# Performance work log

Hardware: AMD Instinct MI355X
Metric: run time of the kernel (lower is better)

## Reference

```python
import jax, jax.numpy as jnp
import numpy as np

WIN = 11
K1 = 0.01
K2 = 0.03


def setup_inputs() -> dict:
    key = jax.random.key(0)
    k1, k2 = jax.random.split(key)
    B, C, H, W = 64, 1, 512, 512
    img = jax.random.uniform(k1, (B, C, H, W), dtype=jnp.float32)
    ref = jax.random.uniform(k2, (B, C, H, W), dtype=jnp.float32)
    data_range = jnp.ones((B,), dtype=jnp.float32)
    return {"img": img, "ref": ref, "data_range": data_range}


def _box_filter(x, win):
    w = jnp.ones((1, 1, win, win), dtype=x.dtype) / (win * win)
    pad = win // 2
    return jax.lax.conv_general_dilated(
        x, w, window_strides=(1, 1),
        padding=[(pad, pad), (pad, pad)],
        dimension_numbers=("NCHW", "OIHW", "NCHW"))


def reference(img, ref, data_range):
    dr = data_range[:, None, None, None]
    C1 = (K1 * dr) ** 2
    C2 = (K2 * dr) ** 2
    n_pix = WIN * WIN
    cov_norm = n_pix / (n_pix - 1)

    ux = _box_filter(img, WIN)
    uy = _box_filter(ref, WIN)
    uxx = _box_filter(img * img, WIN)
    uyy = _box_filter(ref * ref, WIN)
    uxy = _box_filter(img * ref, WIN)

    vx = cov_norm * (uxx - ux * ux)
    vy = cov_norm * (uyy - uy * uy)
    vxy = cov_norm * (uxy - ux * uy)

    A1 = 2 * ux * uy + C1
    A2 = 2 * vxy + C2
    B1 = ux ** 2 + uy ** 2 + C1
    B2 = vx + vy + C2
    S = A1 * A2 / (B1 * B2)
    return S
```

## Files before the change

kernel.cpp:

```cpp
#include <hip/hip_runtime.h>


static constexpr int HI = 512, WI = 512;
static constexpr int RS = 8;
static constexpr int STEPS = RS + 10;
static constexpr int SPB = HI / RS;

struct R8 { float4 a, b; };

__device__ __forceinline__ R8 ld8(const float* p) {
  R8 r; r.a = ((const float4*)p)[0]; r.b = ((const float4*)p)[1]; return r;
}

__device__ __forceinline__ void horiz11(const float v[8], float H[8], int lane) {
  float L[5], R[5];
#pragma unroll
  for (int k = 0; k < 5; ++k) {
    float lt = __shfl(v[3 + k], (lane + 63) & 63);
    L[k] = (lane == 0) ? 0.f : lt;
    float rt = __shfl(v[k], (lane + 1) & 63);
    R[k] = (lane == 63) ? 0.f : rt;
  }
  float h = (((L[0] + L[1]) + (L[2] + L[3])) + ((L[4] + v[0]) + (v[1] + v[2])))
            + ((v[3] + v[4]) + v[5]);
  H[0] = h;
  h = h - L[0] + v[6]; H[1] = h;
  h = h - L[1] + v[7]; H[2] = h;
  h = h - L[2] + R[0]; H[3] = h;
  h = h - L[3] + R[1]; H[4] = h;
  h = h - L[4] + R[2]; H[5] = h;
  h = h - v[0] + R[3]; H[6] = h;
  h = h - v[1] + R[4]; H[7] = h;
}

__global__ __launch_bounds__(256, 2)
void ssim_wave(const float* __restrict__ img, const float* __restrict__ ref,
               const float* __restrict__ drng, const float* __restrict__ zrow,
               float* __restrict__ out)
{
  int bid = (int)blockIdx.x;
  const int nb = (int)gridDim.x;
  if ((nb & 7) == 0) {
    const int cpx = nb >> 3;
    bid = (bid & 7) * cpx + (bid >> 3);
  }

  const int lane = threadIdx.x & 63;
  const int wv   = bid * 4 + (threadIdx.x >> 6);
  const int b    = wv / SPB;
  const int r0   = (wv % SPB) * RS;
  const int c0   = lane * 8;

  const float dr  = drng[b];
  const float C1  = (0.01f * dr) * (0.01f * dr);
  const float C2  = (0.03f * dr) * (0.03f * dr);
  const float inv_n    = 1.0f / 121.0f;
  const float cov_norm = 121.0f / 120.0f;

  const size_t base = (size_t)b * ((size_t)HI * WI);
  const float* xb = img + base;
  const float* yb = ref + base;
  float*       ob = out + base;

  auto nptr = [&](const float* tb, int i) -> const float* {
    const int ri = r0 - 5 + i;
    return (((unsigned)ri < (unsigned)HI) ? tb + (size_t)ri * WI : zrow) + c0;
  };
  auto optr = [&](const float* tb, int i) -> const float* {
    const int ro = r0 - 16 + i;
    return ((i >= 11 && ro >= 0) ? tb + (size_t)ro * WI : zrow) + c0;
  };

  float Sx[8], Sy[8], Sxx[8], Syy[8], Sxy[8];
#pragma unroll
  for (int c = 0; c < 8; ++c) { Sx[c]=0.f; Sy[c]=0.f; Sxx[c]=0.f; Syy[c]=0.f; Sxy[c]=0.f; }

  R8 nx[2], ny[2], ox[2], oy[2];
  nx[0]=ld8(nptr(xb,0)); ny[0]=ld8(nptr(yb,0)); ox[0]=ld8(optr(xb,0)); oy[0]=ld8(optr(yb,0));
  nx[1]=ld8(nptr(xb,1)); ny[1]=ld8(nptr(yb,1)); ox[1]=ld8(optr(xb,1)); oy[1]=ld8(optr(yb,1));

#pragma unroll 2
  for (int i = 0; i < STEPS; ++i) {
    const int s = i & 1;
    float xn[8] = { nx[s].a.x, nx[s].a.y, nx[s].a.z, nx[s].a.w,
                    nx[s].b.x, nx[s].b.y, nx[s].b.z, nx[s].b.w };
    float yn[8] = { ny[s].a.x, ny[s].a.y, ny[s].a.z, ny[s].a.w,
                    ny[s].b.x, ny[s].b.y, ny[s].b.z, ny[s].b.w };
    float xo[8] = { ox[s].a.x, ox[s].a.y, ox[s].a.z, ox[s].a.w,
                    ox[s].b.x, ox[s].b.y, ox[s].b.z, ox[s].b.w };
    float yo[8] = { oy[s].a.x, oy[s].a.y, oy[s].a.z, oy[s].a.w,
                    oy[s].b.x, oy[s].b.y, oy[s].b.z, oy[s].b.w };

    if (i + 2 < STEPS) {
      nx[s]=ld8(nptr(xb,i+2)); ny[s]=ld8(nptr(yb,i+2));
      ox[s]=ld8(optr(xb,i+2)); oy[s]=ld8(optr(yb,i+2));
    }

#pragma unroll
    for (int c = 0; c < 8; ++c) {
      Sx[c]  += xn[c] - xo[c];
      Sy[c]  += yn[c] - yo[c];
      Sxx[c] = fmaf(xn[c], xn[c], fmaf(-xo[c], xo[c], Sxx[c]));
      Syy[c] = fmaf(yn[c], yn[c], fmaf(-yo[c], yo[c], Syy[c]));
      Sxy[c] = fmaf(xn[c], yn[c], fmaf(-xo[c], yo[c], Sxy[c]));
    }

    if (i >= 10) {
      float H0[8], H1[8], H2[8], H3[8], H4[8];
      horiz11(Sx,  H0, lane);
      horiz11(Sy,  H1, lane);
      horiz11(Sxx, H2, lane);
      horiz11(Syy, H3, lane);
      horiz11(Sxy, H4, lane);

      float res[8];
#pragma unroll
      for (int c = 0; c < 8; ++c) {
        const float ux  = H0[c] * inv_n, uy  = H1[c] * inv_n;
        const float uxx = H2[c] * inv_n, uyy = H3[c] * inv_n, uxy = H4[c] * inv_n;
        const float vx  = cov_norm * (uxx - ux * ux);
        const float vy  = cov_norm * (uyy - uy * uy);
        const float vxy = cov_norm * (uxy - ux * uy);
        const float A1 = 2.f * ux * uy + C1;
        const float A2 = 2.f * vxy + C2;
        const float B1 = ux * ux + uy * uy + C1;
        const float B2 = vx + vy + C2;
        res[c] = (A1 * A2) * __builtin_amdgcn_rcpf(B1 * B2);
      }
      const int ro = r0 + i - 10;
      float4* po = (float4*)(ob + (size_t)ro * WI + c0);
      po[0] = make_float4(res[0], res[1], res[2], res[3]);
      po[1] = make_float4(res[4], res[5], res[6], res[7]);
    }
  }
}

extern "C" void kernel_launch(void* const* d_in, const int* in_sizes, int n_in,
                              void* d_out, int out_size, void* d_ws, size_t ws_size,
                              hipStream_t stream)
{
  const float* img = (const float*)d_in[0];
  const float* ref = (const float*)d_in[1];
  const float* drg = (const float*)d_in[2];
  float* out = (float*)d_out;

  hipMemsetAsync(d_ws, 0, (size_t)WI * sizeof(float) + 64, stream);

  const int B = in_sizes[0] / (HI * WI);
  const int waves = B * SPB;
  dim3 grid(waves / 4);
  dim3 block(256);
  hipLaunchKernelGGL(ssim_wave, grid, block, 0, stream,
                     img, ref, drg, (const float*)d_ws, out);
}
```

Baseline: 222.6 us.

## Double rows per wave and peel warm-up loop to skip dummy old-row loads

Each wave now produces 16 output rows instead of 8, so the 10-row vertical halo is amortised over more outputs and less input is re-read per output row. The sliding loop is split into a warm-up phase that only accumulates new rows and a steady phase that adds new rows and subtracts old ones. The warm-up phase no longer loads or subtracts zero rows. The grid is halved, which lowers the number of resident waves for hiding latency, and the peeled loop makes the code larger.

```diff
diff --git a/kernel.cpp b/kernel.cpp
--- a/kernel.cpp
+++ b/kernel.cpp
@@ -2,14 +2,18 @@
 
 
 static constexpr int HI = 512, WI = 512;
-static constexpr int RS = 8;
-static constexpr int STEPS = RS + 10;
+static constexpr int RS = 16;
 static constexpr int SPB = HI / RS;
 
 struct R8 { float4 a, b; };
 
 __device__ __forceinline__ R8 ld8(const float* p) {
   R8 r; r.a = ((const float4*)p)[0]; r.b = ((const float4*)p)[1]; return r;
+}
+
+__device__ __forceinline__ void unp(const R8& v, float o[8]) {
+  o[0]=v.a.x; o[1]=v.a.y; o[2]=v.a.z; o[3]=v.a.w;
+  o[4]=v.b.x; o[5]=v.b.y; o[6]=v.b.z; o[7]=v.b.w;
 }
 
 __device__ __forceinline__ void horiz11(const float v[8], float H[8], int lane) {
@@ -62,77 +66,114 @@
   const float* yb = ref + base;
   float*       ob = out + base;
 
-  auto nptr = [&](const float* tb, int i) -> const float* {
-    const int ri = r0 - 5 + i;
-    return (((unsigned)ri < (unsigned)HI) ? tb + (size_t)ri * WI : zrow) + c0;
+  auto nrow = [&](const float* tb, int t) -> const float* {
+    const int r = r0 - 5 + t;
+    return (((unsigned)r < (unsigned)HI) ? tb + (size_t)r * WI : zrow) + c0;
   };
-  auto optr = [&](const float* tb, int i) -> const float* {
-    const int ro = r0 - 16 + i;
-    return ((i >= 11 && ro >= 0) ? tb + (size_t)ro * WI : zrow) + c0;
+  auto orow = [&](const float* tb, int t) -> const float* {
+    const int r = r0 - 16 + t;
+    return (((unsigned)r < (unsigned)HI) ? tb + (size_t)r * WI : zrow) + c0;
   };
 
   float Sx[8], Sy[8], Sxx[8], Syy[8], Sxy[8];
 #pragma unroll
   for (int c = 0; c < 8; ++c) { Sx[c]=0.f; Sy[c]=0.f; Sxx[c]=0.f; Syy[c]=0.f; Sxy[c]=0.f; }
 
-  R8 nx[2], ny[2], ox[2], oy[2];
-  nx[0]=ld8(nptr(xb,0)); ny[0]=ld8(nptr(yb,0)); ox[0]=ld8(optr(xb,0)); oy[0]=ld8(optr(yb,0));
-  nx[1]=ld8(nptr(xb,1)); ny[1]=ld8(nptr(yb,1)); ox[1]=ld8(optr(xb,1)); oy[1]=ld8(optr(yb,1));
-
-#pragma unroll 2
-  for (int i = 0; i < STEPS; ++i) {
-    const int s = i & 1;
-    float xn[8] = { nx[s].a.x, nx[s].a.y, nx[s].a.z, nx[s].a.w,
-                    nx[s].b.x, nx[s].b.y, nx[s].b.z, nx[s].b.w };
-    float yn[8] = { ny[s].a.x, ny[s].a.y, ny[s].a.z, ny[s].a.w,
-                    ny[s].b.x, ny[s].b.y, ny[s].b.z, ny[s].b.w };
-    float xo[8] = { ox[s].a.x, ox[s].a.y, ox[s].a.z, ox[s].a.w,
-                    ox[s].b.x, ox[s].b.y, ox[s].b.z, ox[s].b.w };
-    float yo[8] = { oy[s].a.x, oy[s].a.y, oy[s].a.z, oy[s].a.w,
-                    oy[s].b.x, oy[s].b.y, oy[s].b.z, oy[s].b.w };
-
-    if (i + 2 < STEPS) {
-      nx[s]=ld8(nptr(xb,i+2)); ny[s]=ld8(nptr(yb,i+2));
-      ox[s]=ld8(optr(xb,i+2)); oy[s]=ld8(optr(yb,i+2));
-    }
-
+  auto accA = [&](const float xn[8], const float yn[8]) {
 #pragma unroll
     for (int c = 0; c < 8; ++c) {
-      Sx[c]  += xn[c] - xo[c];
-      Sy[c]  += yn[c] - yo[c];
+      Sx[c] += xn[c];  Sy[c] += yn[c];
+      Sxx[c] = fmaf(xn[c], xn[c], Sxx[c]);
+      Syy[c] = fmaf(yn[c], yn[c], Syy[c]);
+      Sxy[c] = fmaf(xn[c], yn[c], Sxy[c]);
+    }
+  };
+  auto accB = [&](const float xn[8], const float yn[8],
+                  const float xo[8], const float yo[8]) {
+#pragma unroll
+    for (int c = 0; c < 8; ++c) {
+      Sx[c] += xn[c] - xo[c];
+      Sy[c] += yn[c] - yo[c];
       Sxx[c] = fmaf(xn[c], xn[c], fmaf(-xo[c], xo[c], Sxx[c]));
       Syy[c] = fmaf(yn[c], yn[c], fmaf(-yo[c], yo[c], Syy[c]));
       Sxy[c] = fmaf(xn[c], yn[c], fmaf(-xo[c], yo[c], Sxy[c]));
     }
+  };
 
-    if (i >= 10) {
-      float H0[8], H1[8], H2[8], H3[8], H4[8];
-      horiz11(Sx,  H0, lane);
-      horiz11(Sy,  H1, lane);
-      horiz11(Sxx, H2, lane);
-      horiz11(Syy, H3, lane);
-      horiz11(Sxy, H4, lane);
+  auto emit = [&](int t) {
+    float H0[8], H1[8], H2[8], H3[8], H4[8];
+    horiz11(Sx,  H0, lane);
+    horiz11(Sy,  H1, lane);
+    horiz11(Sxx, H2, lane);
+    horiz11(Syy, H3, lane);
+    horiz11(Sxy, H4, lane);
+    float res[8];
+#pragma unroll
+    for (int c = 0; c < 8; ++c) {
+      const float ux  = H0[c] * inv_n, uy  = H1[c] * inv_n;
+      const float uxx = H2[c] * inv_n, uyy = H3[c] * inv_n, uxy = H4[c] * inv_n;
+      const float vx  = cov_norm * (uxx - ux * ux);
+      const float vy  = cov_norm * (uyy - uy * uy);
+      const float vxy = cov_norm * (uxy - ux * uy);
+      const float A1 = 2.f * ux * uy + C1;
+      const float A2 = 2.f * vxy + C2;
+      const float B1 = ux * ux + uy * uy + C1;
+      const float B2 = vx + vy + C2;
+      res[c] = (A1 * A2) * __builtin_amdgcn_rcpf(B1 * B2);
+    }
+    const int ro = r0 + t - 10;
+    float4* po = (float4*)(ob + (size_t)ro * WI + c0);
+    po[0] = make_float4(res[0], res[1], res[2], res[3]);
+    po[1] = make_float4(res[4], res[5], res[6], res[7]);
+  };
 
-      float res[8];
-#pragma unroll
-      for (int c = 0; c < 8; ++c) {
-        const float ux  = H0[c] * inv_n, uy  = H1[c] * inv_n;
-        const float uxx = H2[c] * inv_n, uyy = H3[c] * inv_n, uxy = H4[c] * inv_n;
-        const float vx  = cov_norm * (uxx - ux * ux);
-        const float vy  = cov_norm * (uyy - uy * uy);
-        const float vxy = cov_norm * (uxy - ux * uy);
-        const float A1 = 2.f * ux * uy + C1;
-        const float A2 = 2.f * vxy + C2;
-        const float B1 = ux * ux + uy * uy + C1;
-        const float B2 = vx + vy + C2;
-        res[c] = (A1 * A2) * __builtin_amdgcn_rcpf(B1 * B2);
-      }
-      const int ro = r0 + i - 10;
-      float4* po = (float4*)(ob + (size_t)ro * WI + c0);
-      po[0] = make_float4(res[0], res[1], res[2], res[3]);
-      po[1] = make_float4(res[4], res[5], res[6], res[7]);
+  R8 nx[2], ny[2], ox[2], oy[2];
+  nx[0] = ld8(nrow(xb, 0)); ny[0] = ld8(nrow(yb, 0));
+  nx[1] = ld8(nrow(xb, 1)); ny[1] = ld8(nrow(yb, 1));
+
+#pragma unroll 2
+  for (int t = 0; t < 9; ++t) {
+    const int s = t & 1;
+    float xn[8], yn[8];
+    unp(nx[s], xn); unp(ny[s], yn);
+    nx[s] = ld8(nrow(xb, t + 2)); ny[s] = ld8(nrow(yb, t + 2));
+    accA(xn, yn);
+  }
+  {
+    float xn[8], yn[8];
+    unp(nx[1], xn); unp(ny[1], yn);
+    nx[1] = ld8(nrow(xb, 11)); ny[1] = ld8(nrow(yb, 11));
+    ox[1] = ld8(orow(xb, 11)); oy[1] = ld8(orow(yb, 11));
+    accA(xn, yn);
+  }
+  {
+    float xn[8], yn[8];
+    unp(nx[0], xn); unp(ny[0], yn);
+    nx[0] = ld8(nrow(xb, 12)); ny[0] = ld8(nrow(yb, 12));
+    ox[0] = ld8(orow(xb, 12)); oy[0] = ld8(orow(yb, 12));
+    accA(xn, yn);
+    emit(10);
+  }
+
+  auto stepB = [&](int t, int s, bool issue) {
+    float xn[8], yn[8], xo[8], yo[8];
+    unp(nx[s], xn); unp(ny[s], yn); unp(ox[s], xo); unp(oy[s], yo);
+    if (issue) {
+      nx[s] = ld8(nrow(xb, t + 2)); ny[s] = ld8(nrow(yb, t + 2));
+      ox[s] = ld8(orow(xb, t + 2)); oy[s] = ld8(orow(yb, t + 2));
     }
+    accB(xn, yn, xo, yo);
+    emit(t);
+  };
+
+#pragma unroll 1
+  for (int u = 0; u < 6; ++u) {
+    stepB(11 + 2 * u, 1, true);
+    stepB(12 + 2 * u, 0, true);
   }
+  stepB(23, 1, true);
+  stepB(24, 0, false);
+  stepB(25, 1, false);
 }
 
 extern "C" void kernel_launch(void* const* d_in, const int* in_sizes, int n_in,
```

Measured after the change: 205.8 us. 7.5% less time.
